# Performance work log

Hardware: AMD Instinct MI355X
Metric: run time of the kernel (lower is better)

The kernel has to match this reference:

```python
import jax, jax.numpy as jnp
import numpy as np


def _gather_neighbours(h, idx):
    # h: (B, N, H); idx: (B, N, K) int -> (B, N, K, H)
    B, N, H = h.shape
    K = idx.shape[-1]
    flat = idx.reshape(B, N * K)  # (B, N*K)
    rep = jnp.take_along_axis(h, flat[..., None], axis=1)  # (B, N*K, H)
    return rep.reshape(B, N, K, H)


def _masked_agg(h, idx, mask):
    # gather neighbor hidden states then masked sum over neighbors -> (B, N, H)
    rep = _gather_neighbours(h, idx)
    return jnp.einsum('bnkh,bnk->bnh', rep, mask)


def setup_inputs() -> dict:
    key = jax.random.key(0)
    ks = jax.random.split(key, 12)
    B, N, H, K = 8, 2000, 128, 32
    s = 1.0 / np.sqrt(H)
    return {
        'node_hidden': jax.random.normal(ks[0], (B, N, H), jnp.float32),
        'cell': jax.random.normal(ks[1], (B, N, H), jnp.float32),
        'w_in': jax.random.normal(ks[2], (4, H, H), jnp.float32) * s,
        'w_out': jax.random.normal(ks[3], (4, H, H), jnp.float32) * s,
        'u_in': jax.random.normal(ks[4], (4, H, H), jnp.float32) * s,
        'u_out': jax.random.normal(ks[5], (4, H, H), jnp.float32) * s,
        'b': jax.random.normal(ks[6], (4, H), jnp.float32) * 0.1,
        'in_node_mask': jax.random.uniform(ks[7], (B, N, K), jnp.float32),
        'out_node_mask': jax.random.uniform(ks[8], (B, N, K), jnp.float32),
        'in_node_index': jax.random.randint(ks[9], (B, N, K), 0, N, jnp.int32),
        'out_node_index': jax.random.randint(ks[10], (B, N, K), 0, N, jnp.int32),
        'layer_num': 2,
    }


def reference(node_hidden, cell, w_in, w_out, u_in, u_out, b,
              in_node_mask, out_node_mask, in_node_index, out_node_index,
              layer_num):
    h, c = node_hidden, cell
    for _ in range(layer_num):
        in_agg = _masked_agg(h, in_node_index, in_node_mask)    # (B,N,H)
        out_agg = _masked_agg(h, out_node_index, out_node_mask)  # (B,N,H)
        # gate pre-activations, gate order: i, o, f, cell
        pre = (jnp.einsum('bnh,ghd->gbnd', in_agg, w_in)
               + jnp.einsum('bnh,ghd->gbnd', out_agg, w_out)
               + jnp.einsum('bnh,ghd->gbnd', h, u_in)
               + jnp.einsum('bnh,ghd->gbnd', h, u_out)
               + b[:, None, None, :])
        i_g = jax.nn.sigmoid(pre[0])
        o_g = jax.nn.sigmoid(pre[1])
        f_g = jax.nn.sigmoid(pre[2])
        g = jnp.tanh(pre[3])
        c = f_g * c + i_g * g
        h = o_g * jnp.tanh(c)
    return h
```

## Files before the change

kernel.cpp:

```cpp
#include <hip/hip_runtime.h>
#include <math.h>

#define B_ 8
#define N_ 2000
#define H_ 128
#define K_ 32
#define M_ (B_*N_)
#define KTOT 384
#define NC 512
#define NTILES 32
#define NCHUNK 12
#define AGG_BLOCKS (M_ / 8)
#define PREP_BLOCKS (NTILES * NCHUNK)
#define GEMM_BLOCKS 1024
#define CH_SH (24 * 512)

typedef __attribute__((ext_vector_type(8))) short s8_t;
typedef __attribute__((ext_vector_type(4))) float f4_t;

__device__ __forceinline__ unsigned short f2bf(float x) {
    union { float f; unsigned u; } v; v.f = x;
    unsigned r = v.u + 0x7fff + ((v.u >> 16) & 1);
    return (unsigned short)(r >> 16);
}
__device__ __forceinline__ float bf2f(unsigned short b) {
    union { unsigned u; float f; } v; v.u = (unsigned)b << 16; return v.f;
}
__device__ __forceinline__ float sigm_(float x) { return 1.f / (1.f + __expf(-x)); }
__device__ __forceinline__ float tanh_(float x) { return 2.f / (1.f + __expf(-2.f * x)) - 1.f; }

__device__ __forceinline__ float pickv(f4_t A, int m) {
    float ab = (m & 1) ? A.y : A.x;
    float cd = (m & 1) ? A.w : A.z;
    return (m & 2) ? cd : ab;
}
__device__ __forceinline__ float pick4(float u0, float u1, float u2, float u3, int m) {
    float ab = (m & 1) ? u1 : u0;
    float cd = (m & 1) ? u3 : u2;
    return (m & 2) ? cd : ab;
}

__device__ __forceinline__ void split4(const float* f, ushort4& hi, ushort4& lo) {
    unsigned short h0 = f2bf(f[0]), h1 = f2bf(f[1]), h2 = f2bf(f[2]), h3 = f2bf(f[3]);
    hi = make_ushort4(h0, h1, h2, h3);
    lo = make_ushort4(f2bf(f[0] - bf2f(h0)), f2bf(f[1] - bf2f(h1)),
                      f2bf(f[2] - bf2f(h2)), f2bf(f[3] - bf2f(h3)));
}

__device__ __forceinline__ void gload_lds(const unsigned short* g, short* l) {
    __builtin_amdgcn_global_load_lds(
        (const __attribute__((address_space(1))) unsigned*)g,
        (__attribute__((address_space(3))) unsigned*)l, 16, 0, 0);
}

__device__ __forceinline__ void prep_elem(int pb, int t,
                                          const float* __restrict__ w_in,
                                          const float* __restrict__ w_out,
                                          const float* __restrict__ u_in,
                                          const float* __restrict__ u_out,
                                          unsigned short* __restrict__ wp_hi,
                                          unsigned short* __restrict__ wp_lo) {
    int ntile = pb / NCHUNK, chunk = pb % NCHUNK;
    int lane = t >> 3, e = t & 7;
    int col = ntile * 16 + (lane & 15);
    int k = chunk * 32 + (lane >> 4) * 8 + e;
    int d = col >> 2, g = col & 3;
    float v;
    if (k < 128) {
        v = w_in[(g * 128 + k) * 128 + d];
    } else if (k < 256) {
        v = w_out[(g * 128 + (k - 128)) * 128 + d];
    } else {
        int kk = k - 256;
        v = u_in[(g * 128 + kk) * 128 + d] + u_out[(g * 128 + kk) * 128 + d];
    }
    unsigned short hs = f2bf(v);
    wp_hi[(size_t)pb * 512 + t] = hs;
    wp_lo[(size_t)pb * 512 + t] = f2bf(v - bf2f(hs));
}

__device__ __forceinline__ void agg_body(int a, int tid,
                                         const float* __restrict__ h,
                                         const int* __restrict__ in_idx,
                                         const float* __restrict__ in_mask,
                                         const int* __restrict__ out_idx,
                                         const float* __restrict__ out_mask,
                                         unsigned short* __restrict__ A_hi,
                                         unsigned short* __restrict__ A_lo,
                                         int (*s_idx)[64], float (*s_msk)[64]) {
    int r = tid >> 5;
    int p = tid & 31;
    int row = a * 8 + r;
    int b = row / N_;
    const float* hb = h + (size_t)b * N_ * H_;

    for (int e = tid; e < 512; e += 256) {
        int r2 = e >> 6, q = e & 63;
        int ridx = a * 8 + r2;
        if (q < 32) {
            s_idx[r2][q] = in_idx[ridx * K_ + q];
            s_msk[r2][q] = in_mask[ridx * K_ + q];
        } else {
            s_idx[r2][q] = out_idx[ridx * K_ + (q - 32)];
            s_msk[r2][q] = out_mask[ridx * K_ + (q - 32)];
        }
    }
    __syncthreads();

    int d0 = p * 4;
    float ai[4] = {0.f, 0.f, 0.f, 0.f};
    float ao[4] = {0.f, 0.f, 0.f, 0.f};
    #pragma unroll 16
    for (int k = 0; k < K_; ++k) {
        int   i1 = s_idx[r][k];
        float m1 = s_msk[r][k];
        int   i2 = s_idx[r][32 + k];
        float m2 = s_msk[r][32 + k];
        float4 v1 = *(const float4*)(hb + (size_t)i1 * H_ + d0);
        float4 v2 = *(const float4*)(hb + (size_t)i2 * H_ + d0);
        ai[0] += m1 * v1.x; ai[1] += m1 * v1.y; ai[2] += m1 * v1.z; ai[3] += m1 * v1.w;
        ao[0] += m2 * v2.x; ao[1] += m2 * v2.y; ao[2] += m2 * v2.z; ao[3] += m2 * v2.w;
    }
    float4 hv4 = *(const float4*)(h + (size_t)row * H_ + d0);
    float hh[4] = {hv4.x, hv4.y, hv4.z, hv4.w};

    int mtile = row >> 4;
    int kg = (p >> 1) & 3;
    int e0 = (p & 1) * 4;
    int lane = (row & 15) + 16 * kg;
    size_t bi = ((size_t)(mtile * NCHUNK +     (p >> 3)) * 64 + lane) * 8 + e0;
    size_t bo = ((size_t)(mtile * NCHUNK + 4 + (p >> 3)) * 64 + lane) * 8 + e0;
    size_t bh = ((size_t)(mtile * NCHUNK + 8 + (p >> 3)) * 64 + lane) * 8 + e0;

    ushort4 hi, lo;
    split4(ai, hi, lo); *(ushort4*)(A_hi + bi) = hi; *(ushort4*)(A_lo + bi) = lo;
    split4(ao, hi, lo); *(ushort4*)(A_hi + bo) = hi; *(ushort4*)(A_lo + bo) = lo;
    split4(hh, hi, lo); *(ushort4*)(A_hi + bh) = hi; *(ushort4*)(A_lo + bh) = lo;
}

__global__ __launch_bounds__(256)
void agg0_prep_kernel(const float* __restrict__ h,
                      const int* __restrict__ in_idx,
                      const float* __restrict__ in_mask,
                      const int* __restrict__ out_idx,
                      const float* __restrict__ out_mask,
                      unsigned short* __restrict__ A_hi,
                      unsigned short* __restrict__ A_lo,
                      const float* __restrict__ w_in,
                      const float* __restrict__ w_out,
                      const float* __restrict__ u_in,
                      const float* __restrict__ u_out,
                      unsigned short* __restrict__ wp_hi,
                      unsigned short* __restrict__ wp_lo) {
    __shared__ int   s_idx[8][64];
    __shared__ float s_msk[8][64];
    int tid = threadIdx.x;
    if (blockIdx.x < AGG_BLOCKS) {
        int bid = (blockIdx.x & 7) * 250 + (blockIdx.x >> 3);
        agg_body(bid, tid, h, in_idx, in_mask, out_idx, out_mask,
                 A_hi, A_lo, s_idx, s_msk);
    } else {
        int pb = blockIdx.x - AGG_BLOCKS;
        prep_elem(pb, tid,       w_in, w_out, u_in, u_out, wp_hi, wp_lo);
        prep_elem(pb, tid + 256, w_in, w_out, u_in, u_out, wp_hi, wp_lo);
    }
}

__global__ __launch_bounds__(256)
void agg_kernel(const float* __restrict__ h,
                const int* __restrict__ in_idx,
                const float* __restrict__ in_mask,
                const int* __restrict__ out_idx,
                const float* __restrict__ out_mask,
                unsigned short* __restrict__ A_hi,
                unsigned short* __restrict__ A_lo) {
    __shared__ int   s_idx[8][64];
    __shared__ float s_msk[8][64];
    int bid = (blockIdx.x & 7) * 250 + (blockIdx.x >> 3);
    agg_body(bid, threadIdx.x, h, in_idx, in_mask, out_idx, out_mask,
             A_hi, A_lo, s_idx, s_msk);
}

__device__ __forceinline__ void frag_load(const short* sb, int wm, int wn, int lane,
                                          s8_t (&ah)[4], s8_t (&al)[4],
                                          s8_t (&bh)[2], s8_t (&bl)[2]) {
    #pragma unroll
    for (int i = 0; i < 4; ++i) {
        ah[i] = *(const s8_t*)&sb[(wm * 4 + i) * 512 + lane * 8];
        al[i] = *(const s8_t*)&sb[(8 + wm * 4 + i) * 512 + lane * 8];
    }
    #pragma unroll
    for (int j = 0; j < 2; ++j) {
        bh[j] = *(const s8_t*)&sb[(16 + wn * 2 + j) * 512 + lane * 8];
        bl[j] = *(const s8_t*)&sb[(20 + wn * 2 + j) * 512 + lane * 8];
    }
}

__device__ __forceinline__ void mfma_chunk(
        const s8_t (&ah)[4], const s8_t (&al)[4],
        const s8_t (&bh)[2], const s8_t (&bl)[2],
        f4_t (&acc)[4][2]) {
    #pragma unroll
    for (int i = 0; i < 4; ++i)
        #pragma unroll
        for (int j = 0; j < 2; ++j) {
            acc[i][j] = __builtin_amdgcn_mfma_f32_16x16x32_bf16(ah[i], bh[j], acc[i][j], 0, 0, 0);
            acc[i][j] = __builtin_amdgcn_mfma_f32_16x16x32_bf16(ah[i], bl[j], acc[i][j], 0, 0, 0);
            acc[i][j] = __builtin_amdgcn_mfma_f32_16x16x32_bf16(al[i], bh[j], acc[i][j], 0, 0, 0);
        }
}

__global__ __launch_bounds__(256, 3)
void gemm_gates(const unsigned short* __restrict__ A_hi,
                const unsigned short* __restrict__ A_lo,
                const unsigned short* __restrict__ wp_hi,
                const unsigned short* __restrict__ wp_lo,
                const float* __restrict__ bias,
                const float* __restrict__ c_src,
                float* __restrict__ c_dst,
                float* __restrict__ h_dst,
                int write_c) {
    __shared__ short sL[2 * CH_SH];
    int l = blockIdx.x;
    int x = l & 7;
    int s_slot = l >> 3;
    int mt_lo  = x ? ((2000 * x + 63) >> 7) : 0;
    int mt_nxt = (2000 * (x + 1) + 63) >> 7;
    int cnt = (mt_nxt - mt_lo) * 8;
    if (s_slot >= cnt) return;
    int mt = mt_lo + (s_slot >> 3);
    int jt = s_slot & 7;

    int tid  = threadIdx.x;
    int lane = tid & 63;
    int w    = tid >> 6;
    int wm   = w & 1;
    int wn   = w >> 1;
    int mtile0 = mt * 8;
    int ntile0 = jt * 4;

    const unsigned short* gp[6];
    short* lpA[6];
    short* lpB[6];
    #pragma unroll
    for (int i = 0; i < 6; ++i) {
        int s = i * 4 + w;
        const unsigned short* src;
        if (s < 8)       src = A_hi  + ((size_t)((mtile0 + s)      * NCHUNK) * 64 + lane) * 8;
        else if (s < 16) src = A_lo  + ((size_t)((mtile0 + s - 8)  * NCHUNK) * 64 + lane) * 8;
        else if (s < 20) src = wp_hi + ((size_t)((ntile0 + s - 16) * NCHUNK) * 64 + lane) * 8;
        else             src = wp_lo + ((size_t)((ntile0 + s - 20) * NCHUNK) * 64 + lane) * 8;
        gp[i] = src;
        lpA[i] = &sL[s * 512];
        lpB[i] = &sL[CH_SH + s * 512];
    }

    f4_t zero = {0.f, 0.f, 0.f, 0.f};
    f4_t acc[4][2];
    #pragma unroll
    for (int i = 0; i < 4; ++i)
        #pragma unroll
        for (int j = 0; j < 2; ++j) acc[i][j] = zero;

    s8_t ah[4], al[4], bh[2], bl[2];

    #pragma unroll
    for (int i = 0; i < 6; ++i) { gload_lds(gp[i], lpA[i]); gp[i] += 512; }

    #pragma unroll 1
    for (int c = 0; c < NCHUNK; c += 2) {
        if (c + 1 < NCHUNK) {
            #pragma unroll
            for (int i = 0; i < 6; ++i) { gload_lds(gp[i], lpB[i]); gp[i] += 512; }
            asm volatile("s_waitcnt vmcnt(6)" ::: "memory");
        } else {
            asm volatile("s_waitcnt vmcnt(0)" ::: "memory");
        }
        asm volatile("s_barrier" ::: "memory");
        frag_load(sL, wm, wn, lane, ah, al, bh, bl);
        asm volatile("s_waitcnt lgkmcnt(0)" ::: "memory");
        __builtin_amdgcn_sched_barrier(0);
        asm volatile("s_barrier" ::: "memory");
        mfma_chunk(ah, al, bh, bl, acc);

        if (c + 2 < NCHUNK) {
            #pragma unroll
            for (int i = 0; i < 6; ++i) { gload_lds(gp[i], lpA[i]); gp[i] += 512; }
            asm volatile("s_waitcnt vmcnt(6)" ::: "memory");
        } else {
            asm volatile("s_waitcnt vmcnt(0)" ::: "memory");
        }
        asm volatile("s_barrier" ::: "memory");
        frag_load(sL + CH_SH, wm, wn, lane, ah, al, bh, bl);
        asm volatile("s_waitcnt lgkmcnt(0)" ::: "memory");
        __builtin_amdgcn_sched_barrier(0);
        asm volatile("s_barrier" ::: "memory");
        mfma_chunk(ah, al, bh, bl, acc);
    }

    int g    = lane & 3;
    int qrow = lane >> 4;
    int dl   = (lane >> 2) & 3;
    #pragma unroll
    for (int j = 0; j < 2; ++j) {
        int ncol_base = jt * 64 + wn * 32 + j * 16;
        int d = (ncol_base >> 2) + dl;
        float b0 = bias[0 * 128 + d];
        float b1 = bias[1 * 128 + d];
        float b2 = bias[2 * 128 + d];
        float b3 = bias[3 * 128 + d];
        #pragma unroll
        for (int i = 0; i < 4; ++i) {
            f4_t A = acc[i][j];
            float s0 = pickv(A, g);
            float s1 = pickv(A, g ^ 1);
            float s2 = pickv(A, g ^ 2);
            float s3 = pickv(A, g ^ 3);
            float u0 = s0;
            float u1 = __shfl_xor(s1, 1);
            float u2 = __shfl_xor(s2, 2);
            float u3 = __shfl_xor(s3, 3);
            float p0 = pick4(u0, u1, u2, u3, g) + b0;
            float p1 = pick4(u0, u1, u2, u3, g ^ 1) + b1;
            float p2 = pick4(u0, u1, u2, u3, g ^ 2) + b2;
            float p3 = pick4(u0, u1, u2, u3, g ^ 3) + b3;
            float ig = sigm_(p0);
            float og = sigm_(p1);
            float fg = sigm_(p2);
            float cg = tanh_(p3);
            int row = mt * 128 + wm * 64 + i * 16 + qrow * 4 + g;
            size_t off = (size_t)row * H_ + d;
            float c_old = c_src[off];
            float c_new = fg * c_old + ig * cg;
            if (write_c) c_dst[off] = c_new;
            h_dst[off] = og * tanh_(c_new);
        }
    }
}

extern "C" void kernel_launch(void* const* d_in, const int* in_sizes, int n_in,
                              void* d_out, int out_size, void* d_ws, size_t ws_size,
                              hipStream_t stream) {
    const float* node_hidden = (const float*)d_in[0];
    const float* cell        = (const float*)d_in[1];
    const float* w_in        = (const float*)d_in[2];
    const float* w_out       = (const float*)d_in[3];
    const float* u_in        = (const float*)d_in[4];
    const float* u_out       = (const float*)d_in[5];
    const float* bias        = (const float*)d_in[6];
    const float* in_mask     = (const float*)d_in[7];
    const float* out_mask    = (const float*)d_in[8];
    const int*   in_idx      = (const int*)d_in[9];
    const int*   out_idx     = (const int*)d_in[10];
    float* out = (float*)d_out;

    char* p = (char*)d_ws;
    unsigned short* wp_hi = (unsigned short*)p; p += (size_t)NTILES * NCHUNK * 512 * 2;
    unsigned short* wp_lo = (unsigned short*)p; p += (size_t)NTILES * NCHUNK * 512 * 2;
    unsigned short* A_hi  = (unsigned short*)p; p += (size_t)(M_/16) * NCHUNK * 512 * 2;
    unsigned short* A_lo  = (unsigned short*)p; p += (size_t)(M_/16) * NCHUNK * 512 * 2;
    float* h_buf = (float*)p;                   p += (size_t)M_ * H_ * 4;

    agg0_prep_kernel<<<AGG_BLOCKS + PREP_BLOCKS, 256, 0, stream>>>(
        node_hidden, in_idx, in_mask, out_idx, out_mask, A_hi, A_lo,
        w_in, w_out, u_in, u_out, wp_hi, wp_lo);
    gemm_gates<<<GEMM_BLOCKS, 256, 0, stream>>>(
        A_hi, A_lo, wp_hi, wp_lo, bias, cell, out, h_buf, 1);

    agg_kernel<<<AGG_BLOCKS, 256, 0, stream>>>(h_buf, in_idx, in_mask,
                                               out_idx, out_mask, A_hi, A_lo);
    gemm_gates<<<GEMM_BLOCKS, 256, 0, stream>>>(
        A_hi, A_lo, wp_hi, wp_lo, bias, out, out, out, 0);
}
```

Before: 185.3 us.

## Restructure aggregation to 4 rows per block with wave-shuffle index broadcast

The gather-aggregate kernel now handles 4 rows per block, one wavefront per row. Each half of the wave accumulates either the in or the out neighbour sum, which halves the per-thread gather chain and doubles the block count. Index and mask values are loaded into registers and broadcast with shuffles, replacing the shared-memory staging and the __syncthreads. Loads and stores use nontemporal hints. In exchange, each block carries twice as many threads per row and does more shuffle work.

Measured after the change: 219.7 us. 18.6% more time.

```diff
diff --git a/kernel.cpp b/kernel.cpp
--- a/kernel.cpp
+++ b/kernel.cpp
@@ -10,13 +10,14 @@
 #define NC 512
 #define NTILES 32
 #define NCHUNK 12
-#define AGG_BLOCKS (M_ / 8)
+#define AGG_BLOCKS (M_ / 4)
 #define PREP_BLOCKS (NTILES * NCHUNK)
 #define GEMM_BLOCKS 1024
 #define CH_SH (24 * 512)
 
 typedef __attribute__((ext_vector_type(8))) short s8_t;
 typedef __attribute__((ext_vector_type(4))) float f4_t;
+typedef __attribute__((ext_vector_type(4))) unsigned short us4_t;
 
 __device__ __forceinline__ unsigned short f2bf(float x) {
     union { float f; unsigned u; } v; v.f = x;
@@ -40,11 +41,11 @@
     return (m & 2) ? cd : ab;
 }
 
-__device__ __forceinline__ void split4(const float* f, ushort4& hi, ushort4& lo) {
+__device__ __forceinline__ void split4(const float* f, us4_t& hi, us4_t& lo) {
     unsigned short h0 = f2bf(f[0]), h1 = f2bf(f[1]), h2 = f2bf(f[2]), h3 = f2bf(f[3]);
-    hi = make_ushort4(h0, h1, h2, h3);
-    lo = make_ushort4(f2bf(f[0] - bf2f(h0)), f2bf(f[1] - bf2f(h1)),
-                      f2bf(f[2] - bf2f(h2)), f2bf(f[3] - bf2f(h3)));
+    hi = (us4_t){h0, h1, h2, h3};
+    lo = (us4_t){f2bf(f[0] - bf2f(h0)), f2bf(f[1] - bf2f(h1)),
+                 f2bf(f[2] - bf2f(h2)), f2bf(f[3] - bf2f(h3))};
 }
 
 __device__ __forceinline__ void gload_lds(const unsigned short* g, short* l) {
@@ -86,56 +87,56 @@
                                          const int* __restrict__ out_idx,
                                          const float* __restrict__ out_mask,
                                          unsigned short* __restrict__ A_hi,
-                                         unsigned short* __restrict__ A_lo,
-                                         int (*s_idx)[64], float (*s_msk)[64]) {
-    int r = tid >> 5;
-    int p = tid & 31;
-    int row = a * 8 + r;
+                                         unsigned short* __restrict__ A_lo) {
+    int r = tid >> 6;
+    int q = tid & 63;
+    int row = a * 4 + r;
     int b = row / N_;
     const float* hb = h + (size_t)b * N_ * H_;
 
-    for (int e = tid; e < 512; e += 256) {
-        int r2 = e >> 6, q = e & 63;
-        int ridx = a * 8 + r2;
-        if (q < 32) {
-            s_idx[r2][q] = in_idx[ridx * K_ + q];
-            s_msk[r2][q] = in_mask[ridx * K_ + q];
-        } else {
-            s_idx[r2][q] = out_idx[ridx * K_ + (q - 32)];
-            s_msk[r2][q] = out_mask[ridx * K_ + (q - 32)];
-        }
-    }
-    __syncthreads();
-
+    int   idxreg;
+    float mskreg;
+    if (q < 32) {
+        idxreg = __builtin_nontemporal_load(&in_idx[row * K_ + q]);
+        mskreg = __builtin_nontemporal_load(&in_mask[row * K_ + q]);
+    } else {
+        idxreg = __builtin_nontemporal_load(&out_idx[row * K_ + (q - 32)]);
+        mskreg = __builtin_nontemporal_load(&out_mask[row * K_ + (q - 32)]);
+    }
+
+    int p = q & 31;
     int d0 = p * 4;
-    float ai[4] = {0.f, 0.f, 0.f, 0.f};
-    float ao[4] = {0.f, 0.f, 0.f, 0.f};
+    int kbase = (q >> 5) * 32;
+    float acc4[4] = {0.f, 0.f, 0.f, 0.f};
     #pragma unroll 16
     for (int k = 0; k < K_; ++k) {
-        int   i1 = s_idx[r][k];
-        float m1 = s_msk[r][k];
-        int   i2 = s_idx[r][32 + k];
-        float m2 = s_msk[r][32 + k];
-        float4 v1 = *(const float4*)(hb + (size_t)i1 * H_ + d0);
-        float4 v2 = *(const float4*)(hb + (size_t)i2 * H_ + d0);
-        ai[0] += m1 * v1.x; ai[1] += m1 * v1.y; ai[2] += m1 * v1.z; ai[3] += m1 * v1.w;
-        ao[0] += m2 * v2.x; ao[1] += m2 * v2.y; ao[2] += m2 * v2.z; ao[3] += m2 * v2.w;
-    }
-    float4 hv4 = *(const float4*)(h + (size_t)row * H_ + d0);
-    float hh[4] = {hv4.x, hv4.y, hv4.z, hv4.w};
+        int   i1 = __shfl(idxreg, kbase + k);
+        float m1 = __shfl(mskreg, kbase + k);
+        float4 v = *(const float4*)(hb + (size_t)i1 * H_ + d0);
+        acc4[0] += m1 * v.x; acc4[1] += m1 * v.y;
+        acc4[2] += m1 * v.z; acc4[3] += m1 * v.w;
+    }
 
     int mtile = row >> 4;
     int kg = (p >> 1) & 3;
     int e0 = (p & 1) * 4;
     int lane = (row & 15) + 16 * kg;
-    size_t bi = ((size_t)(mtile * NCHUNK +     (p >> 3)) * 64 + lane) * 8 + e0;
-    size_t bo = ((size_t)(mtile * NCHUNK + 4 + (p >> 3)) * 64 + lane) * 8 + e0;
-    size_t bh = ((size_t)(mtile * NCHUNK + 8 + (p >> 3)) * 64 + lane) * 8 + e0;
-
-    ushort4 hi, lo;
-    split4(ai, hi, lo); *(ushort4*)(A_hi + bi) = hi; *(ushort4*)(A_lo + bi) = lo;
-    split4(ao, hi, lo); *(ushort4*)(A_hi + bo) = hi; *(ushort4*)(A_lo + bo) = lo;
-    split4(hh, hi, lo); *(ushort4*)(A_hi + bh) = hi; *(ushort4*)(A_lo + bh) = lo;
+    int slotbase = (q >= 32) ? 4 : 0;
+    size_t boff = ((size_t)(mtile * NCHUNK + slotbase + (p >> 3)) * 64 + lane) * 8 + e0;
+
+    us4_t hi, lo;
+    split4(acc4, hi, lo);
+    __builtin_nontemporal_store(hi, (us4_t*)(A_hi + boff));
+    __builtin_nontemporal_store(lo, (us4_t*)(A_lo + boff));
+
+    if (q < 32) {
+        float4 hv4 = *(const float4*)(h + (size_t)row * H_ + d0);
+        float hh[4] = {hv4.x, hv4.y, hv4.z, hv4.w};
+        size_t bh = ((size_t)(mtile * NCHUNK + 8 + (p >> 3)) * 64 + lane) * 8 + e0;
+        split4(hh, hi, lo);
+        __builtin_nontemporal_store(hi, (us4_t*)(A_hi + bh));
+        __builtin_nontemporal_store(lo, (us4_t*)(A_lo + bh));
+    }
 }
 
 __global__ __launch_bounds__(256)
@@ -152,13 +153,10 @@
                       const float* __restrict__ u_out,
                       unsigned short* __restrict__ wp_hi,
                       unsigned short* __restrict__ wp_lo) {
-    __shared__ int   s_idx[8][64];
-    __shared__ float s_msk[8][64];
     int tid = threadIdx.x;
     if (blockIdx.x < AGG_BLOCKS) {
-        int bid = (blockIdx.x & 7) * 250 + (blockIdx.x >> 3);
-        agg_body(bid, tid, h, in_idx, in_mask, out_idx, out_mask,
-                 A_hi, A_lo, s_idx, s_msk);
+        int bid = (blockIdx.x & 7) * 500 + (blockIdx.x >> 3);
+        agg_body(bid, tid, h, in_idx, in_mask, out_idx, out_mask, A_hi, A_lo);
     } else {
         int pb = blockIdx.x - AGG_BLOCKS;
         prep_elem(pb, tid,       w_in, w_out, u_in, u_out, wp_hi, wp_lo);
@@ -174,11 +172,8 @@
                 const float* __restrict__ out_mask,
                 unsigned short* __restrict__ A_hi,
                 unsigned short* __restrict__ A_lo) {
-    __shared__ int   s_idx[8][64];
-    __shared__ float s_msk[8][64];
-    int bid = (blockIdx.x & 7) * 250 + (blockIdx.x >> 3);
-    agg_body(bid, threadIdx.x, h, in_idx, in_mask, out_idx, out_mask,
-             A_hi, A_lo, s_idx, s_msk);
+    int bid = (blockIdx.x & 7) * 500 + (blockIdx.x >> 3);
+    agg_body(bid, threadIdx.x, h, in_idx, in_mask, out_idx, out_mask, A_hi, A_lo);
 }
 
 __device__ __forceinline__ void frag_load(const short* sb, int wm, int wn, int lane,
```
